# Kernel optimization log

Measured on AMD Instinct MI355X. Metric: run time of the kernel, lower is better.

## Reference

```python
import jax, jax.numpy as jnp
import numpy as np

B, L, D, H, FD, NL, NV, NN, MAXSPD = 2, 1024, 1024, 16, 512, 4, 5000, 5000, 30
DF = 4 * D
S = L + 2  # 1 graph token + 1 sos token + L data tokens
DH = D // H
NEG = -1e9  # finite stand-in for -inf query mask (constant per softmax row -> same probs, no NaNs)


def rmsnorm(x, w, eps=1e-6):
    return x * jax.lax.rsqrt(jnp.mean(x * x, axis=-1, keepdims=True) + eps) * w


def setup_inputs() -> dict:
    key = jax.random.key(0)
    ks = jax.random.split(key, 24)
    f = lambda k, sh, s=0.02: (jax.random.normal(k, sh, jnp.float32) * s)
    return {
        "graph_features": jax.random.normal(ks[0], (B, 1, D), jnp.float32),
        "input_features": jax.random.normal(ks[1], (B, L, FD), jnp.float32),
        "proj_W": f(ks[2], (FD, D)),
        "proj_b": jnp.zeros((D,), jnp.float32),
        "sos_token": f(ks[3], (1, 1, D)),
        "node_emb": f(ks[4], (NN, D)),
        "type_emb": f(ks[5], (2, D)),
        "pos_emb": f(ks[6], (S, D)),
        "spd_emb": f(ks[7], (MAXSPD + 2, H)),
        "attn_norm_w": jnp.ones((NL, D), jnp.float32),
        "wq": f(ks[8], (NL, D, D)),
        "wk": f(ks[9], (NL, D, D)),
        "wv": f(ks[10], (NL, D, D)),
        "wo": f(ks[11], (NL, D, D)),
        "ffn_norm_w": jnp.ones((NL, D), jnp.float32),
        "w1": f(ks[12], (NL, D, DF)),
        "w2": f(ks[13], (NL, DF, D)),
        "w3": f(ks[14], (NL, D, DF)),
        "final_norm_w": jnp.ones((D,), jnp.float32),
        "out_W": f(ks[15], (D, NV)),
        "out_b": jnp.zeros((NV,), jnp.float32),
        "subnode_ids": jax.random.randint(ks[16], (B, L), 0, NN),
        "token_mask_len": jax.random.randint(ks[17], (B,), 1, L),
        "spd_indices": jax.random.randint(ks[18], (B, L, L), 0, MAXSPD + 1),
        "start_pos": 0,
    }


def reference(graph_features, input_features, proj_W, proj_b, sos_token, node_emb,
              type_emb, pos_emb, spd_emb, attn_norm_w, wq, wk, wv, wo, ffn_norm_w,
              w1, w2, w3, final_norm_w, out_W, out_b,
              subnode_ids, token_mask_len, spd_indices, start_pos):
    bsz = input_features.shape[0]
    glen = graph_features.shape[1]  # 1

    # token embedding fusion
    h_data = input_features @ proj_W + proj_b                      # [B,L,D]
    sos = jnp.broadcast_to(sos_token, (bsz, 1, D))
    h_tokens = jnp.concatenate([sos, h_data], axis=1)              # [B,L+1,D]
    sub_ext = jnp.concatenate([jnp.zeros((bsz, 1), subnode_ids.dtype), subnode_ids], axis=1)
    h_tokens = h_tokens + node_emb[sub_ext] + type_emb[0]
    h_graph = graph_features + type_emb[1]
    h = jnp.concatenate([h_graph, h_tokens], axis=1)               # [B,S,D]
    seqlen = h.shape[1]

    # SPD relative bias -> [B,H,S,S]
    max_spd = spd_emb.shape[0] - 2
    full_spd = jnp.full((bsz, seqlen, seqlen), max_spd + 1, dtype=jnp.int32)
    full_spd = full_spd.at[:, 2:, 2:].set(spd_indices.astype(jnp.int32))
    full_spd = full_spd.at[:, 0, 0].set(0).at[:, 1, 1].set(0)
    graph_bias = jnp.transpose(spd_emb[full_spd], (0, 3, 1, 2))

    h = h + pos_emb[:seqlen]

    # additive query-validity mask [B,1,S,1] broadcast over keys
    positions = jnp.arange(seqlen)[None, :]
    valid = positions < (token_mask_len[:, None] + 1 + glen)
    mask = jnp.where(valid, 0.0, NEG).astype(h.dtype)[:, None, :, None]

    scale = 1.0 / np.sqrt(DH)
    n_heads = graph_bias.shape[1]
    for i in range(wq.shape[0]):
        x = rmsnorm(h, attn_norm_w[i])
        q = (x @ wq[i]).reshape(bsz, seqlen, n_heads, DH)
        k = (x @ wk[i]).reshape(bsz, seqlen, n_heads, DH)
        v = (x @ wv[i]).reshape(bsz, seqlen, n_heads, DH)
        scores = jnp.einsum('bqhd,bkhd->bhqk', q, k) * scale + graph_bias + mask
        p = jax.nn.softmax(scores, axis=-1)
        att = jnp.einsum('bhqk,bkhd->bqhd', p, v).reshape(bsz, seqlen, D) @ wo[i]
        h = h + att
        x2 = rmsnorm(h, ffn_norm_w[i])
        h = h + (jax.nn.silu(x2 @ w1[i]) * (x2 @ w3[i])) @ w2[i]

    h = rmsnorm(h, final_norm_w)
    h_seq = h[:, glen:, :]                                          # [B,L+1,D]
    return (h_seq @ out_W + out_b).astype(jnp.float32)
```

## Files before the change

### kernel.cpp

```cpp
#include <hip/hip_runtime.h>

#define DMODEL 1024
#define DFF    4096
#define NHEAD  16
#define DHEAD  64
#define LTOK   1024
#define SEQ    1026
#define SPAD   1088
#define MPAD   2176
#define NVOC   5000
#define NVOCP  5120
#define MOUT   2050

typedef float  floatx4 __attribute__((ext_vector_type(4)));
typedef __bf16 bf16x8  __attribute__((ext_vector_type(8)));

__device__ __forceinline__ unsigned short f2b(float f) {
  unsigned int u = __builtin_bit_cast(unsigned int, f);
  u += 0x7FFFu + ((u >> 16) & 1u);
  return (unsigned short)(u >> 16);
}
__device__ __forceinline__ float b2f(unsigned short v) {
  return __builtin_bit_cast(float, ((unsigned int)v) << 16);
}
__device__ __forceinline__ void gl2lds16(const void* g, void* l) {
  __builtin_amdgcn_global_load_lds((const __attribute__((address_space(1))) void*)g,
                                   (__attribute__((address_space(3))) void*)l, 16, 0, 0);
}
__device__ __forceinline__ floatx4 mfma16(bf16x8 a, bf16x8 b, floatx4 c) {
  return __builtin_amdgcn_mfma_f32_16x16x32_bf16(a, b, c, 0, 0, 0);
}

__global__ __launch_bounds__(256) void f2b_kernel(const float* __restrict__ s,
                                                  unsigned short* __restrict__ d, int n) {
  int i = (blockIdx.x * 256 + threadIdx.x) * 4;
  if (i >= n) return;
  float4 v = *(const float4*)(s + i);
  ushort4 o; o.x = f2b(v.x); o.y = f2b(v.y); o.z = f2b(v.z); o.w = f2b(v.w);
  *(ushort4*)(d + i) = o;
}

__global__ __launch_bounds__(256) void transconv_kernel(
    const float* __restrict__ p0, const float* __restrict__ p1,
    const float* __restrict__ p2, const float* __restrict__ p3,
    unsigned short* __restrict__ dst, long dstZ, int R, int C) {
  const float* src = (blockIdx.z == 0) ? p0 : (blockIdx.z == 1) ? p1 : (blockIdx.z == 2) ? p2 : p3;
  dst += dstZ * blockIdx.z;
  __shared__ float T[64][68];
  const int r0 = blockIdx.y * 64, c0 = blockIdx.x * 64;
  const int tr = threadIdx.x >> 4, tc = threadIdx.x & 15;
#pragma unroll
  for (int it = 0; it < 4; it++) {
    int rl = tr + it * 16;
    int cg = c0 + tc * 4;
    float4 v = {0.f, 0.f, 0.f, 0.f};
    if (cg < C) v = *(const float4*)(src + (size_t)(r0 + rl) * C + cg);
    T[rl][tc * 4 + 0] = v.x; T[rl][tc * 4 + 1] = v.y;
    T[rl][tc * 4 + 2] = v.z; T[rl][tc * 4 + 3] = v.w;
  }
  __syncthreads();
#pragma unroll
  for (int it = 0; it < 4; it++) {
    int ol = tr + it * 16;
    int oc = c0 + ol;
    if (oc < C) {
      ushort4 o;
      o.x = f2b(T[tc * 4 + 0][ol]); o.y = f2b(T[tc * 4 + 1][ol]);
      o.z = f2b(T[tc * 4 + 2][ol]); o.w = f2b(T[tc * 4 + 3][ol]);
      *(ushort4*)(dst + (size_t)oc * R + r0 + tc * 4) = o;
    }
  }
}

__global__ __launch_bounds__(256) void build_h_kernel(
    float* __restrict__ h, const float* __restrict__ gf, const float* __restrict__ sos,
    const float* __restrict__ nodeE, const float* __restrict__ typeE,
    const float* __restrict__ posE, const int* __restrict__ sub) {
  const int s = blockIdx.x, b = blockIdx.y;
  const int c = threadIdx.x * 4;
  float* o = h + ((size_t)(b * SPAD + s)) * DMODEL + c;
  if (s >= SEQ) { o[0] = 0.f; o[1] = 0.f; o[2] = 0.f; o[3] = 0.f; return; }
  float4 p = *(const float4*)(posE + (size_t)s * DMODEL + c);
  if (s == 0) {
    float4 g = *(const float4*)(gf + (size_t)b * DMODEL + c);
    float4 t = *(const float4*)(typeE + DMODEL + c);
    o[0] = g.x + t.x + p.x; o[1] = g.y + t.y + p.y;
    o[2] = g.z + t.z + p.z; o[3] = g.w + t.w + p.w;
  } else {
    float4 t = *(const float4*)(typeE + c);
    int nid = (s == 1) ? 0 : sub[b * LTOK + s - 2];
    float4 ne = *(const float4*)(nodeE + (size_t)nid * DMODEL + c);
    if (s == 1) {
      float4 ss = *(const float4*)(sos + c);
      o[0] = ss.x + ne.x + t.x + p.x; o[1] = ss.y + ne.y + t.y + p.y;
      o[2] = ss.z + ne.z + t.z + p.z; o[3] = ss.w + ne.w + t.w + p.w;
    } else {
      o[0] += ne.x + t.x + p.x; o[1] += ne.y + t.y + p.y;
      o[2] += ne.z + t.z + p.z; o[3] += ne.w + t.w + p.w;
    }
  }
}

__global__ __launch_bounds__(256) void rmsnorm_kernel(const float* __restrict__ h,
                                                      const float* __restrict__ w,
                                                      unsigned short* __restrict__ out,
                                                      int final_mode) {
  const int r = blockIdx.x;
  int srow = r;
  if (final_mode) {
    if (r >= MOUT) {
      ushort4 z = {0, 0, 0, 0};
      *(ushort4*)(out + (size_t)r * DMODEL + threadIdx.x * 4) = z;
      return;
    }
    int b = r / 1025;
    srow = b * SPAD + 1 + (r - b * 1025);
  }
  float4 x = *(const float4*)(h + (size_t)srow * DMODEL + threadIdx.x * 4);
  float ss = x.x * x.x + x.y * x.y + x.z * x.z + x.w * x.w;
#pragma unroll
  for (int off = 32; off > 0; off >>= 1) ss += __shfl_down(ss, off);
  __shared__ float red[4];
  if ((threadIdx.x & 63) == 0) red[threadIdx.x >> 6] = ss;
  __syncthreads();
  float rs = rsqrtf((red[0] + red[1] + red[2] + red[3]) * (1.f / 1024.f) + 1e-6f);
  float4 ww = *(const float4*)(w + threadIdx.x * 4);
  ushort4 o;
  o.x = f2b(x.x * rs * ww.x); o.y = f2b(x.y * rs * ww.y);
  o.z = f2b(x.z * rs * ww.z); o.w = f2b(x.w * rs * ww.w);
  *(ushort4*)(out + (size_t)r * DMODEL + threadIdx.x * 4) = o;
}

__global__ __launch_bounds__(320) void bidx_kernel(const int* __restrict__ spd,
                                                   unsigned char* __restrict__ bidx) {
  const int qg = blockIdx.x, b = blockIdx.y;
  const int k0 = threadIdx.x * 4;
  if (k0 >= SPAD) return;
  uchar4 o;
  unsigned char v[4];
#pragma unroll
  for (int j = 0; j < 4; j++) {
    int kg = k0 + j;
    if (qg >= SEQ || kg >= SEQ) {
      v[j] = 32;
    } else if (qg >= 2 && kg >= 2) {
      int idx = spd[((size_t)b * LTOK + (qg - 2)) * LTOK + (kg - 2)];
      v[j] = (unsigned char)(idx < 0 ? 0 : (idx > 31 ? 31 : idx));
    } else {
      v[j] = (qg == kg) ? 0 : 31;
    }
  }
  o.x = v[0]; o.y = v[1]; o.z = v[2]; o.w = v[3];
  *(uchar4*)(bidx + ((size_t)b * SPAD + qg) * SPAD + k0) = o;
}

__global__ __launch_bounds__(256) void vtrans_kernel(const unsigned short* __restrict__ v,
                                                     unsigned short* __restrict__ vt) {
  const int st = blockIdx.x, hh = blockIdx.y, b = blockIdx.z;
  __shared__ unsigned short T[64][72];
  const int tr = threadIdx.x >> 4, tc = threadIdx.x & 15;
#pragma unroll
  for (int it = 0; it < 4; it++) {
    int r = tr + it * 16;
    ushort4 val = *(const ushort4*)(v + ((size_t)(b * SPAD + st * 64 + r)) * DMODEL + hh * DHEAD + tc * 4);
    T[r][tc * 4 + 0] = val.x; T[r][tc * 4 + 1] = val.y;
    T[r][tc * 4 + 2] = val.z; T[r][tc * 4 + 3] = val.w;
  }
  __syncthreads();
#pragma unroll
  for (int it = 0; it < 4; it++) {
    int d = tr + it * 16;
    ushort4 o;
    o.x = T[tc * 4 + 0][d]; o.y = T[tc * 4 + 1][d];
    o.z = T[tc * 4 + 2][d]; o.w = T[tc * 4 + 3][d];
    *(ushort4*)(vt + (((size_t)(b * NHEAD + hh)) * DHEAD + d) * SPAD + st * 64 + tc * 4) = o;
  }
}

#define PST 80
__global__ __launch_bounds__(256) void attn_kernel(
    const unsigned short* __restrict__ qb, const unsigned short* __restrict__ kb,
    const unsigned short* __restrict__ vt, unsigned short* __restrict__ attb,
    const float* __restrict__ spdE, const unsigned char* __restrict__ bidx,
    const int* __restrict__ tml) {
  const int qt = blockIdx.x, hh = blockIdx.y, bb = blockIdx.z;
  const int tid = threadIdx.x;
  const int w = tid >> 6, lane = tid & 63;
  const int quad = lane >> 4, l16 = lane & 15;

  __shared__ unsigned short Qs[64 * PST];
  __shared__ unsigned short Ks[64 * PST];
  __shared__ unsigned short Vts[64 * PST];
  __shared__ unsigned short Ps[4 * 16 * PST];
  __shared__ unsigned char Is[64 * 64];
  __shared__ float bias_tab[33];

  if (tid < 33) bias_tab[tid] = (tid < 32) ? spdE[tid * NHEAD + hh] : -3.0e38f;

#pragma unroll
  for (int jj = 0; jj < 2; jj++) {
    int c = tid + (jj << 8);
    int r = c >> 3, ch = c & 7;
    int4 val = *(const int4*)(qb + ((size_t)(bb * SPAD + qt * 64 + r)) * DMODEL + hh * DHEAD + ch * 8);
    *(int4*)(Qs + r * PST + ch * 8) = val;
  }
  const int tmlb = tml[bb];

  const int sr = tid >> 3, sch = tid & 7;
  const int ir = tid >> 2, ic = (tid & 3) * 16;
  int4 kreg[2], vreg[2], ireg;
  {
    const int kt = 0;
#pragma unroll
    for (int jj = 0; jj < 2; jj++) {
      int r = sr + jj * 32;
      kreg[jj] = *(const int4*)(kb + ((size_t)(bb * SPAD + kt * 64 + r)) * DMODEL + hh * DHEAD + sch * 8);
      vreg[jj] = *(const int4*)(vt + (((size_t)(bb * NHEAD + hh)) * DHEAD + r) * SPAD + kt * 64 + sch * 8);
    }
    ireg = *(const int4*)(bidx + ((size_t)bb * SPAD + qt * 64 + ir) * SPAD + kt * 64 + ic);
  }
  __syncthreads();

  bf16x8 aq[2];
  aq[0] = *(const bf16x8*)(Qs + (w * 16 + l16) * PST + quad * 8);
  aq[1] = *(const bf16x8*)(Qs + (w * 16 + l16) * PST + 32 + quad * 8);

  floatx4 O[4];
  float m_i[4], l_i[4];
#pragma unroll
  for (int d = 0; d < 4; d++) { floatx4 z = {0.f, 0.f, 0.f, 0.f}; O[d] = z; }
#pragma unroll
  for (int r = 0; r < 4; r++) { m_i[r] = -3.0e38f; l_i[r] = 0.f; }

  unsigned short* PsW = Ps + w * 16 * PST;
  float maskv[4];
#pragma unroll
  for (int r = 0; r < 4; r++) {
    int qg = qt * 64 + w * 16 + quad * 4 + r;
    maskv[r] = (qg < tmlb + 2) ? 0.f : -1.0e9f;
  }

  for (int kt = 0; kt < 17; kt++) {
#pragma unroll
    for (int jj = 0; jj < 2; jj++) {
      int r = sr + jj * 32;
      *(int4*)(Ks + r * PST + sch * 8) = kreg[jj];
      *(int4*)(Vts + r * PST + sch * 8) = vreg[jj];
    }
    *(int4*)(Is + ir * 64 + ic) = ireg;
    __syncthreads();

    if (kt < 16) {
      const int kn = kt + 1;
#pragma unroll
      for (int jj = 0; jj < 2; jj++) {
        int r = sr + jj * 32;
        kreg[jj] = *(const int4*)(kb + ((size_t)(bb * SPAD + kn * 64 + r)) * DMODEL + hh * DHEAD + sch * 8);
        vreg[jj] = *(const int4*)(vt + (((size_t)(bb * NHEAD + hh)) * DHEAD + r) * SPAD + kn * 64 + sch * 8);
      }
      ireg = *(const int4*)(bidx + ((size_t)bb * SPAD + qt * 64 + ir) * SPAD + kn * 64 + ic);
    }

    float sc[4][4];
#pragma unroll
    for (int ns = 0; ns < 4; ns++) {
      bf16x8 bk0 = *(const bf16x8*)(Ks + (ns * 16 + l16) * PST + quad * 8);
      bf16x8 bk1 = *(const bf16x8*)(Ks + (ns * 16 + l16) * PST + 32 + quad * 8);
      floatx4 c4 = {0.f, 0.f, 0.f, 0.f};
      c4 = mfma16(aq[0], bk0, c4);
      c4 = mfma16(aq[1], bk1, c4);
#pragma unroll
      for (int r = 0; r < 4; r++) sc[ns][r] = c4[r];
    }

#pragma unroll
    for (int r = 0; r < 4; r++) {
      const unsigned char* isrow = Is + (w * 16 + quad * 4 + r) * 64;
#pragma unroll
      for (int ns = 0; ns < 4; ns++) {
        int idx = isrow[ns * 16 + l16];
        sc[ns][r] = sc[ns][r] * 0.125f + bias_tab[idx] + maskv[r];
      }
    }

    float alpha[4];
#pragma unroll
    for (int r = 0; r < 4; r++) {
      float mx = fmaxf(fmaxf(sc[0][r], sc[1][r]), fmaxf(sc[2][r], sc[3][r]));
#pragma unroll
      for (int off = 1; off < 16; off <<= 1) mx = fmaxf(mx, __shfl_xor(mx, off));
      float mn = fmaxf(m_i[r], mx);
      alpha[r] = __expf(m_i[r] - mn);
      m_i[r] = mn;
      float rs = 0.f;
#pragma unroll
      for (int ns = 0; ns < 4; ns++) { float p = __expf(sc[ns][r] - mn); sc[ns][r] = p; rs += p; }
#pragma unroll
      for (int off = 1; off < 16; off <<= 1) rs += __shfl_xor(rs, off);
      l_i[r] = l_i[r] * alpha[r] + rs;
    }

#pragma unroll
    for (int ns = 0; ns < 4; ns++)
#pragma unroll
      for (int r = 0; r < 4; r++)
        PsW[(quad * 4 + r) * PST + ns * 16 + l16] = f2b(sc[ns][r]);

#pragma unroll
    for (int d = 0; d < 4; d++)
#pragma unroll
      for (int r = 0; r < 4; r++) O[d][r] *= alpha[r];

    bf16x8 ap0 = *(const bf16x8*)(PsW + l16 * PST + quad * 8);
    bf16x8 ap1 = *(const bf16x8*)(PsW + l16 * PST + 32 + quad * 8);
#pragma unroll
    for (int d = 0; d < 4; d++) {
      bf16x8 bv0 = *(const bf16x8*)(Vts + (d * 16 + l16) * PST + quad * 8);
      bf16x8 bv1 = *(const bf16x8*)(Vts + (d * 16 + l16) * PST + 32 + quad * 8);
      O[d] = mfma16(ap0, bv0, O[d]);
      O[d] = mfma16(ap1, bv1, O[d]);
    }
    __syncthreads();
  }

#pragma unroll
  for (int r = 0; r < 4; r++) {
    int qg = qt * 64 + w * 16 + quad * 4 + r;
    float inv = 1.0f / l_i[r];
#pragma unroll
    for (int d = 0; d < 4; d++)
      attb[((size_t)(bb * SPAD + qg)) * DMODEL + hh * DHEAD + d * 16 + l16] = f2b(O[d][r] * inv);
  }
}

__global__ __launch_bounds__(256) void silumul_kernel(const unsigned short* __restrict__ u,
                                                      unsigned short* __restrict__ g, int n) {
  int i = (blockIdx.x * 256 + threadIdx.x) * 4;
  if (i >= n) return;
  const unsigned short* u3 = u + n;
  ushort4 a = *(const ushort4*)(u + i);
  ushort4 c = *(const ushort4*)(u3 + i);
  ushort4 o;
  float x, y;
  x = b2f(a.x); y = b2f(c.x); o.x = f2b(x / (1.f + __expf(-x)) * y);
  x = b2f(a.y); y = b2f(c.y); o.y = f2b(x / (1.f + __expf(-x)) * y);
  x = b2f(a.z); y = b2f(c.z); o.z = f2b(x / (1.f + __expf(-x)) * y);
  x = b2f(a.w); y = b2f(c.w); o.w = f2b(x / (1.f + __expf(-x)) * y);
  *(ushort4*)(g + i) = o;
}

enum { EPI_BF16 = 0, EPI_RESID = 1, EPI_PROJ = 2, EPI_OUT = 3, EPI_ATOMIC = 4 };

template <int EPI>
__global__ __launch_bounds__(256) void gemm_bt_kernel(
    const unsigned short* __restrict__ A, const unsigned short* __restrict__ Bt,
    void* __restrict__ Cv, const float* __restrict__ bias,
    int M, int N, int K, int ld, long zA, long zB, long zC, int Mreal, int Nreal) {
  A += zA * blockIdx.z;
  Bt += zB * blockIdx.z;
  char* Cb = (char*)Cv + zC * blockIdx.z;

  const int tid = threadIdx.x;
  const int lane = tid & 63, wave = tid >> 6;
  const int quad = lane >> 4, l16 = lane & 15;
  const int wr = wave >> 1, wc = wave & 1;
  const int m0 = blockIdx.y << 7, n0 = blockIdx.x << 7;

  __shared__ unsigned short As[128 * 32];
  __shared__ unsigned short Bs[128 * 32];

  floatx4 acc[4][4];
  {
    floatx4 z = {0.f, 0.f, 0.f, 0.f};
#pragma unroll
    for (int i = 0; i < 4; i++)
#pragma unroll
      for (int j = 0; j < 4; j++) acc[i][j] = z;
  }

  for (int k0 = 0; k0 < K; k0 += 32) {
#pragma unroll
    for (int jj = 0; jj < 2; jj++) {
      int c = tid + (jj << 8);
      int r = c >> 2, kc = c & 3;
      gl2lds16(A + (size_t)(m0 + r) * ld + k0 + kc * 8, As + c * 8);
      gl2lds16(Bt + (size_t)(n0 + r) * ld + k0 + kc * 8, Bs + c * 8);
    }
    __syncthreads();
    bf16x8 a[4], b[4];
#pragma unroll
    for (int i = 0; i < 4; i++) a[i] = *(const bf16x8*)(As + (wr * 64 + i * 16 + l16) * 32 + quad * 8);
#pragma unroll
    for (int j = 0; j < 4; j++) b[j] = *(const bf16x8*)(Bs + (wc * 64 + j * 16 + l16) * 32 + quad * 8);
#pragma unroll
    for (int i = 0; i < 4; i++)
#pragma unroll
      for (int j = 0; j < 4; j++) acc[i][j] = mfma16(a[i], b[j], acc[i][j]);
    __syncthreads();
  }

#pragma unroll
  for (int i = 0; i < 4; i++) {
    const int rb = m0 + wr * 64 + i * 16 + quad * 4;
#pragma unroll
    for (int j = 0; j < 4; j++) {
      const int col = n0 + wc * 64 + j * 16 + l16;
#pragma unroll
      for (int r = 0; r < 4; r++) {
        const int row = rb + r;
        float v = acc[i][j][r];
        if constexpr (EPI == EPI_BF16) {
          ((unsigned short*)Cb)[(size_t)row * N + col] = f2b(v);
        } else if constexpr (EPI == EPI_RESID) {
          float* C = (float*)Cb;
          C[(size_t)row * N + col] += v;
        } else if constexpr (EPI == EPI_PROJ) {
          float* C = (float*)Cb;
          int rr = (row >> 10) * SPAD + 2 + (row & 1023);
          C[(size_t)rr * N + col] = v + bias[col];
        } else if constexpr (EPI == EPI_ATOMIC) {
          atomicAdd(&((float*)Cb)[(size_t)row * N + col], v);
        } else {
          if (row < Mreal && col < Nreal)
            ((float*)Cb)[(size_t)row * Nreal + col] = v + bias[col];
        }
      }
    }
  }
}

extern "C" void kernel_launch(void* const* d_in, const int* in_sizes, int n_in,
                              void* d_out, int out_size, void* d_ws, size_t ws_size,
                              hipStream_t stream) {
  const float* gf    = (const float*)d_in[0];
  const float* inpf  = (const float*)d_in[1];
  const float* projW = (const float*)d_in[2];
  const float* projB = (const float*)d_in[3];
  const float* sos   = (const float*)d_in[4];
  const float* nodeE = (const float*)d_in[5];
  const float* typeE = (const float*)d_in[6];
  const float* posE  = (const float*)d_in[7];
  const float* spdE  = (const float*)d_in[8];
  const float* attnW = (const float*)d_in[9];
  const float* wq    = (const float*)d_in[10];
  const float* wk    = (const float*)d_in[11];
  const float* wv    = (const float*)d_in[12];
  const float* wo    = (const float*)d_in[13];
  const float* ffnW  = (const float*)d_in[14];
  const float* w1    = (const float*)d_in[15];
  const float* w2    = (const float*)d_in[16];
  const float* w3    = (const float*)d_in[17];
  const float* finW  = (const float*)d_in[18];
  const float* outW  = (const float*)d_in[19];
  const float* outB  = (const float*)d_in[20];
  const int*   sub   = (const int*)d_in[21];
  const int*   tml   = (const int*)d_in[22];
  const int*   spd   = (const int*)d_in[23];
  float* out = (float*)d_out;
  (void)in_sizes; (void)n_in; (void)out_size; (void)ws_size;

  char* ws = (char*)d_ws;
  constexpr size_t OFF_H     = 0;
  constexpr size_t OFF_XB    = 8912896;
  constexpr size_t OFF_Q     = 13369344;
  constexpr size_t OFF_K     = 17825792;
  constexpr size_t OFF_V     = 22282240;
  constexpr size_t OFF_VT    = 26738688;
  constexpr size_t OFF_ATT   = 31195136;
  constexpr size_t OFF_U     = 35651584;
  constexpr size_t OFF_G     = 71303168;
  constexpr size_t OFF_XF    = 89128960;
  constexpr size_t OFF_INB   = 93585408;
  constexpr size_t OFF_PROJT = 95682560;
  constexpr size_t OFF_OUTWT = 96731136;
  constexpr size_t OFF_SLAB  = 107216896;

  float*          h    = (float*)(ws + OFF_H);
  unsigned short* xb   = (unsigned short*)(ws + OFF_XB);
  unsigned short* qbuf = (unsigned short*)(ws + OFF_Q);
  unsigned short* kbuf = (unsigned short*)(ws + OFF_K);
  unsigned short* vbuf = (unsigned short*)(ws + OFF_V);
  unsigned short* vtb  = (unsigned short*)(ws + OFF_VT);
  unsigned short* attb = (unsigned short*)(ws + OFF_ATT);
  unsigned short* ubuf = (unsigned short*)(ws + OFF_U);
  unsigned short* gbuf = (unsigned short*)(ws + OFF_G);
  unsigned short* xf   = (unsigned short*)(ws + OFF_XF);
  unsigned char*  bidx = (unsigned char*)(ws + OFF_XF);
  unsigned short* inb  = (unsigned short*)(ws + OFF_INB);
  unsigned short* projT = (unsigned short*)(ws + OFF_PROJT);
  unsigned short* outWT = (unsigned short*)(ws + OFF_OUTWT);
  unsigned short* slab  = (unsigned short*)(ws + OFF_SLAB);

  const long DD = (long)DMODEL * DMODEL;
  const long DDF = (long)DMODEL * DFF;
  const long ZC_TOK = (long)MPAD * DMODEL * 2;
  const long ZC_FF  = (long)MPAD * DFF * 2;

  f2b_kernel<<<1024, 256, 0, stream>>>(inpf, inb, 2048 * 512);
  transconv_kernel<<<dim3(16, 8, 1), 256, 0, stream>>>(projW, projW, projW, projW, projT, 0, 512, 1024);
  transconv_kernel<<<dim3(79, 16, 1), 256, 0, stream>>>(outW, outW, outW, outW, outWT, 0, 1024, NVOC);
  bidx_kernel<<<dim3(SPAD, 2), 320, 0, stream>>>(spd, bidx);

  gemm_bt_kernel<EPI_PROJ><<<dim3(8, 16, 1), 256, 0, stream>>>(
      inb, projT, h, projB, 2048, 1024, 512, 512, 0, 0, 0, 0, 0);
  build_h_kernel<<<dim3(SPAD, 2), 256, 0, stream>>>(h, gf, sos, nodeE, typeE, posE, sub);

  for (int i = 0; i < 4; i++) {
    transconv_kernel<<<dim3(16, 16, 4), 256, 0, stream>>>(
        wq + (long)i * DD, wk + (long)i * DD, wv + (long)i * DD, wo + (long)i * DD,
        slab, DD, 1024, 1024);
    transconv_kernel<<<dim3(64, 16, 2), 256, 0, stream>>>(
        w1 + (long)i * DDF, w3 + (long)i * DDF, w1, w1,
        slab + 4 * DD, DDF, 1024, 4096);
    transconv_kernel<<<dim3(16, 64, 1), 256, 0, stream>>>(
        w2 + (long)i * DDF, w2, w2, w2,
        slab + 12 * DD, 0, 4096, 1024);

    rmsnorm_kernel<<<MPAD, 256, 0, stream>>>(h, attnW + i * DMODEL, xb, 0);
    gemm_bt_kernel<EPI_BF16><<<dim3(8, 17, 3), 256, 0, stream>>>(
        xb, slab, qbuf, nullptr, MPAD, 1024, 1024, 1024, 0, DD, ZC_TOK, 0, 0);
    vtrans_kernel<<<dim3(17, 16, 2), 256, 0, stream>>>(vbuf, vtb);
    attn_kernel<<<dim3(17, 16, 2), 256, 0, stream>>>(qbuf, kbuf, vtb, attb, spdE, bidx, tml);
    gemm_bt_kernel<EPI_ATOMIC><<<dim3(8, 17, 2), 256, 0, stream>>>(
        attb, slab + 3 * DD, h, nullptr, MPAD, 1024, 512, 1024, 512, 512, 0, 0, 0);

    rmsnorm_kernel<<<MPAD, 256, 0, stream>>>(h, ffnW + i * DMODEL, xb, 0);
    gemm_bt_kernel<EPI_BF16><<<dim3(32, 17, 2), 256, 0, stream>>>(
        xb, slab + 4 * DD, ubuf, nullptr, MPAD, 4096, 1024, 1024, 0, DDF, ZC_FF, 0, 0);
    silumul_kernel<<<8704, 256, 0, stream>>>(ubuf, gbuf, MPAD * DFF);
    gemm_bt_kernel<EPI_ATOMIC><<<dim3(8, 17, 4), 256, 0, stream>>>(
        gbuf, slab + 12 * DD, h, nullptr, MPAD, 1024, 1024, 4096, 1024, 1024, 0, 0, 0);
  }

  rmsnorm_kernel<<<MPAD, 256, 0, stream>>>(h, finW, xf, 1);
  gemm_bt_kernel<EPI_OUT><<<dim3(40, 17, 1), 256, 0, stream>>>(
      xf, outWT, out, outB, MPAD, NVOCP, 1024, 1024, 0, 0, 0, MOUT, NVOC);
}
```

Before: 1.598 ms.

## Enlarge attention query tile to 128 rows and pack bias indices per lane

The attention kernel now uses 512 threads and 128 query rows per block, so each K/V tile loaded from global memory serves twice as many queries. Heads and batch are folded into one grid dimension. The bias-index precompute writes bytes in a lane-interleaved order, so each lane fetches its four indices with one 32-bit LDS read instead of four byte reads. Because 1088 rows do not divide evenly into 128-row tiles, the last tile clamps its loads and skips stores for out-of-range rows, at the cost of some wasted compute and fewer, larger blocks.

```diff
diff --git a/kernel.cpp b/kernel.cpp
--- a/kernel.cpp
+++ b/kernel.cpp
@@ -134,24 +134,26 @@
 __global__ __launch_bounds__(320) void bidx_kernel(const int* __restrict__ spd,
                                                    unsigned char* __restrict__ bidx) {
   const int qg = blockIdx.x, b = blockIdx.y;
-  const int k0 = threadIdx.x * 4;
-  if (k0 >= SPAD) return;
-  uchar4 o;
+  const int i0 = threadIdx.x * 4;
+  if (i0 >= SPAD) return;
+  const int g = i0 >> 6, c = (i0 >> 2) & 15;
   unsigned char v[4];
 #pragma unroll
-  for (int j = 0; j < 4; j++) {
-    int kg = k0 + j;
+  for (int n = 0; n < 4; n++) {
+    int kg = g * 64 + n * 16 + c;
+    unsigned char vv;
     if (qg >= SEQ || kg >= SEQ) {
-      v[j] = 32;
+      vv = 32;
     } else if (qg >= 2 && kg >= 2) {
       int idx = spd[((size_t)b * LTOK + (qg - 2)) * LTOK + (kg - 2)];
-      v[j] = (unsigned char)(idx < 0 ? 0 : (idx > 31 ? 31 : idx));
+      vv = (unsigned char)(idx < 0 ? 0 : (idx > 31 ? 31 : idx));
     } else {
-      v[j] = (qg == kg) ? 0 : 31;
-    }
-  }
-  o.x = v[0]; o.y = v[1]; o.z = v[2]; o.w = v[3];
-  *(uchar4*)(bidx + ((size_t)b * SPAD + qg) * SPAD + k0) = o;
+      vv = (qg == kg) ? 0 : 31;
+    }
+    v[n] = vv;
+  }
+  uchar4 o; o.x = v[0]; o.y = v[1]; o.z = v[2]; o.w = v[3];
+  *(uchar4*)(bidx + ((size_t)b * SPAD + qg) * SPAD + i0) = o;
 }
 
 __global__ __launch_bounds__(256) void vtrans_kernel(const unsigned short* __restrict__ v,
@@ -178,47 +180,44 @@
 }
 
 #define PST 80
-__global__ __launch_bounds__(256) void attn_kernel(
+__global__ __launch_bounds__(512) void attn_kernel(
     const unsigned short* __restrict__ qb, const unsigned short* __restrict__ kb,
     const unsigned short* __restrict__ vt, unsigned short* __restrict__ attb,
     const float* __restrict__ spdE, const unsigned char* __restrict__ bidx,
     const int* __restrict__ tml) {
-  const int qt = blockIdx.x, hh = blockIdx.y, bb = blockIdx.z;
+  const int hb = blockIdx.x;
+  const int qt = blockIdx.y;
+  const int hh = hb >> 1, bb = hb & 1;
   const int tid = threadIdx.x;
   const int w = tid >> 6, lane = tid & 63;
   const int quad = lane >> 4, l16 = lane & 15;
 
-  __shared__ unsigned short Qs[64 * PST];
+  __shared__ unsigned short Qs[128 * PST];
   __shared__ unsigned short Ks[64 * PST];
   __shared__ unsigned short Vts[64 * PST];
-  __shared__ unsigned short Ps[4 * 16 * PST];
-  __shared__ unsigned char Is[64 * 64];
+  __shared__ unsigned short Ps[8 * 16 * PST];
+  __shared__ unsigned char Is[128 * 64];
   __shared__ float bias_tab[33];
 
   if (tid < 33) bias_tab[tid] = (tid < 32) ? spdE[tid * NHEAD + hh] : -3.0e38f;
 
 #pragma unroll
   for (int jj = 0; jj < 2; jj++) {
-    int c = tid + (jj << 8);
+    int c = tid + (jj << 9);
     int r = c >> 3, ch = c & 7;
-    int4 val = *(const int4*)(qb + ((size_t)(bb * SPAD + qt * 64 + r)) * DMODEL + hh * DHEAD + ch * 8);
+    int qrow = qt * 128 + r; qrow = qrow < SPAD ? qrow : SPAD - 1;
+    int4 val = *(const int4*)(qb + ((size_t)(bb * SPAD + qrow)) * DMODEL + hh * DHEAD + ch * 8);
     *(int4*)(Qs + r * PST + ch * 8) = val;
   }
   const int tmlb = tml[bb];
 
   const int sr = tid >> 3, sch = tid & 7;
   const int ir = tid >> 2, ic = (tid & 3) * 16;
-  int4 kreg[2], vreg[2], ireg;
-  {
-    const int kt = 0;
-#pragma unroll
-    for (int jj = 0; jj < 2; jj++) {
-      int r = sr + jj * 32;
-      kreg[jj] = *(const int4*)(kb + ((size_t)(bb * SPAD + kt * 64 + r)) * DMODEL + hh * DHEAD + sch * 8);
-      vreg[jj] = *(const int4*)(vt + (((size_t)(bb * NHEAD + hh)) * DHEAD + r) * SPAD + kt * 64 + sch * 8);
-    }
-    ireg = *(const int4*)(bidx + ((size_t)bb * SPAD + qt * 64 + ir) * SPAD + kt * 64 + ic);
-  }
+  const int irow = min(qt * 128 + ir, SPAD - 1);
+  int4 kreg, vreg, ireg;
+  kreg = *(const int4*)(kb + ((size_t)(bb * SPAD + sr)) * DMODEL + hh * DHEAD + sch * 8);
+  vreg = *(const int4*)(vt + (((size_t)(bb * NHEAD + hh)) * DHEAD + sr) * SPAD + sch * 8);
+  ireg = *(const int4*)(bidx + ((size_t)bb * SPAD + irow) * SPAD + ic);
   __syncthreads();
 
   bf16x8 aq[2];
@@ -236,29 +235,21 @@
   float maskv[4];
 #pragma unroll
   for (int r = 0; r < 4; r++) {
-    int qg = qt * 64 + w * 16 + quad * 4 + r;
+    int qg = qt * 128 + w * 16 + quad * 4 + r;
     maskv[r] = (qg < tmlb + 2) ? 0.f : -1.0e9f;
   }
 
   for (int kt = 0; kt < 17; kt++) {
-#pragma unroll
-    for (int jj = 0; jj < 2; jj++) {
-      int r = sr + jj * 32;
-      *(int4*)(Ks + r * PST + sch * 8) = kreg[jj];
-      *(int4*)(Vts + r * PST + sch * 8) = vreg[jj];
-    }
+    *(int4*)(Ks + sr * PST + sch * 8) = kreg;
+    *(int4*)(Vts + sr * PST + sch * 8) = vreg;
     *(int4*)(Is + ir * 64 + ic) = ireg;
     __syncthreads();
 
     if (kt < 16) {
       const int kn = kt + 1;
-#pragma unroll
-      for (int jj = 0; jj < 2; jj++) {
-        int r = sr + jj * 32;
-        kreg[jj] = *(const int4*)(kb + ((size_t)(bb * SPAD + kn * 64 + r)) * DMODEL + hh * DHEAD + sch * 8);
-        vreg[jj] = *(const int4*)(vt + (((size_t)(bb * NHEAD + hh)) * DHEAD + r) * SPAD + kn * 64 + sch * 8);
-      }
-      ireg = *(const int4*)(bidx + ((size_t)bb * SPAD + qt * 64 + ir) * SPAD + kn * 64 + ic);
+      kreg = *(const int4*)(kb + ((size_t)(bb * SPAD + kn * 64 + sr)) * DMODEL + hh * DHEAD + sch * 8);
+      vreg = *(const int4*)(vt + (((size_t)(bb * NHEAD + hh)) * DHEAD + sr) * SPAD + kn * 64 + sch * 8);
+      ireg = *(const int4*)(bidx + ((size_t)bb * SPAD + irow) * SPAD + kn * 64 + ic);
     }
 
     float sc[4][4];
@@ -275,10 +266,11 @@
 
 #pragma unroll
     for (int r = 0; r < 4; r++) {
-      const unsigned char* isrow = Is + (w * 16 + quad * 4 + r) * 64;
+      int row = w * 16 + quad * 4 + r;
+      unsigned int iw = *(const unsigned int*)(Is + row * 64 + l16 * 4);
 #pragma unroll
       for (int ns = 0; ns < 4; ns++) {
-        int idx = isrow[ns * 16 + l16];
+        int idx = (iw >> (8 * ns)) & 0xff;
         sc[ns][r] = sc[ns][r] * 0.125f + bias_tab[idx] + maskv[r];
       }
     }
@@ -325,11 +317,13 @@
 
 #pragma unroll
   for (int r = 0; r < 4; r++) {
-    int qg = qt * 64 + w * 16 + quad * 4 + r;
-    float inv = 1.0f / l_i[r];
-#pragma unroll
-    for (int d = 0; d < 4; d++)
-      attb[((size_t)(bb * SPAD + qg)) * DMODEL + hh * DHEAD + d * 16 + l16] = f2b(O[d][r] * inv);
+    int qg = qt * 128 + w * 16 + quad * 4 + r;
+    if (qg < SPAD) {
+      float inv = 1.0f / l_i[r];
+#pragma unroll
+      for (int d = 0; d < 4; d++)
+        attb[((size_t)(bb * SPAD + qg)) * DMODEL + hh * DHEAD + d * 16 + l16] = f2b(O[d][r] * inv);
+    }
   }
 }
 
@@ -520,7 +514,7 @@
     gemm_bt_kernel<EPI_BF16><<<dim3(8, 17, 3), 256, 0, stream>>>(
         xb, slab, qbuf, nullptr, MPAD, 1024, 1024, 1024, 0, DD, ZC_TOK, 0, 0);
     vtrans_kernel<<<dim3(17, 16, 2), 256, 0, stream>>>(vbuf, vtb);
-    attn_kernel<<<dim3(17, 16, 2), 256, 0, stream>>>(qbuf, kbuf, vtb, attb, spdE, bidx, tml);
+    attn_kernel<<<dim3(32, 9, 1), 512, 0, stream>>>(qbuf, kbuf, vtb, attb, spdE, bidx, tml);
     gemm_bt_kernel<EPI_ATOMIC><<<dim3(8, 17, 2), 256, 0, stream>>>(
         attb, slab + 3 * DD, h, nullptr, MPAD, 1024, 512, 1024, 512, 512, 0, 0, 0);
 
```

New measurement: 1.466 ms. 8.3% less time.
